# Kernel tuning notes

Measured on AMD Instinct MI355X. Metric: run time of the kernel, lower is better.

## Reference

```python
import jax, jax.numpy as jnp
import numpy as np

DECAY = 0.6
GAIN = 0.4
LN_EPS = 1e-5


def ema_scan(x, axis):
    # s_t = DECAY*s_{t-1} + GAIN*x_t, s_{-1}=0, along `axis`; vectorized over all other dims
    xm = jnp.moveaxis(x, axis, 0)
    def step(s, xt):
        s = DECAY * s + GAIN * xt
        return s, s
    _, ys = jax.lax.scan(step, jnp.zeros_like(xm[0]), xm)
    return jnp.moveaxis(ys, 0, axis)


def setup_inputs() -> dict:
    key = jax.random.key(0)
    ks = jax.random.split(key, 8)
    B, H, W, D = 8, 96, 96, 192
    C = 2 * D  # inner_dim
    s_in = 1.0 / np.sqrt(D)
    s_out = 1.0 / np.sqrt(C)
    return {
        "x": jax.random.normal(ks[0], (B, H, W, D), dtype=jnp.float32),
        "W_in": jax.random.uniform(ks[1], (D, C), minval=-s_in, maxval=s_in, dtype=jnp.float32),
        "b_in": jax.random.uniform(ks[2], (C,), minval=-s_in, maxval=s_in, dtype=jnp.float32),
        "conv_w": jax.random.uniform(ks[3], (C, 1, 3, 3), minval=-1.0/3.0, maxval=1.0/3.0, dtype=jnp.float32),
        "ln_g": jnp.ones((C,), dtype=jnp.float32),
        "ln_b": jnp.zeros((C,), dtype=jnp.float32),
        "W_out": jax.random.uniform(ks[4], (C, D), minval=-s_out, maxval=s_out, dtype=jnp.float32),
        "b_out": jax.random.uniform(ks[5], (D,), minval=-s_out, maxval=s_out, dtype=jnp.float32),
    }


def reference(x, W_in, b_in, conv_w, ln_g, ln_b, W_out, b_out):
    C = W_in.shape[1]
    # in_proj: [B,H,W,D] -> [B,H,W,C]
    proj = jnp.einsum("bhwd,dc->bhwc", x, W_in) + b_in
    # channels-first for depthwise conv: [B,C,H,W]
    cf = jnp.transpose(proj, (0, 3, 1, 2))
    local = jax.lax.conv_general_dilated(
        cf, conv_w, window_strides=(1, 1), padding="SAME",
        feature_group_count=C,
        dimension_numbers=("NCHW", "OIHW", "NCHW"))
    # four directional EMA scans
    lr = ema_scan(local, 3)
    rl = jnp.flip(ema_scan(jnp.flip(local, 3), 3), 3)
    tb = ema_scan(local, 2)
    bt = jnp.flip(ema_scan(jnp.flip(local, 2), 2), 2)
    mixed = 0.25 * (lr + rl + tb + bt) + local
    # back to channels-last, layernorm over C
    mixed = jnp.transpose(mixed, (0, 2, 3, 1))
    mu = jnp.mean(mixed, axis=-1, keepdims=True)
    var = jnp.mean(jnp.square(mixed - mu), axis=-1, keepdims=True)
    normed = (mixed - mu) * jax.lax.rsqrt(var + LN_EPS) * ln_g + ln_b
    return jnp.einsum("bhwc,cd->bhwd", normed, W_out) + b_out
```

## Files before the change

### kernel.cpp

```cpp
#include <hip/hip_runtime.h>
#include <hip/hip_bf16.h>

#define NB 8
#define NH 96
#define NW 96
#define ND 192
#define NC 384
#define NPOS (NB*NH*NW)

#define DECAY 0.6f
#define GAIN 0.4f
#define D12 2.1767823e-3f
#define D16 2.8211099e-4f
#define D24 4.7383813e-6f

typedef __attribute__((ext_vector_type(8))) short bf16x8;
typedef __attribute__((ext_vector_type(4))) float f32x4;
typedef __attribute__((ext_vector_type(4))) unsigned short us4;

__device__ inline unsigned short f2bf(float f) {
  unsigned u = __float_as_uint(f);
  u += 0x7fff + ((u >> 16) & 1);
  return (unsigned short)(u >> 16);
}
__device__ inline float bf2f(unsigned short u) {
  return __uint_as_float((unsigned)u << 16);
}

__device__ inline void gload16(const void* g, void* l) {
  __builtin_amdgcn_global_load_lds(
      (const __attribute__((address_space(1))) void*)g,
      (__attribute__((address_space(3))) void*)l, 16, 0, 0);
}

__device__ inline f32x4 ldf4(const float* p) {
  return *reinterpret_cast<const f32x4*>(p);
}
__device__ inline f32x4 ldb4(const unsigned short* p) {
  us4 v = *reinterpret_cast<const us4*>(p);
  return (f32x4){bf2f(v.x), bf2f(v.y), bf2f(v.z), bf2f(v.w)};
}
__device__ inline void stb4(unsigned short* p, f32x4 v) {
  us4 o = {f2bf(v[0]), f2bf(v[1]), f2bf(v[2]), f2bf(v[3])};
  *reinterpret_cast<us4*>(p) = o;
}
__device__ inline uint2 pk4(f32x4 v) {
  us4 o = {f2bf(v[0]), f2bf(v[1]), f2bf(v[2]), f2bf(v[3])};
  uint2 r; __builtin_memcpy(&r, &o, 8); return r;
}
__device__ inline f32x4 up4(uint2 p) {
  return (f32x4){__uint_as_float(p.x << 16), __uint_as_float(p.x & 0xffff0000u),
                 __uint_as_float(p.y << 16), __uint_as_float(p.y & 0xffff0000u)};
}
__device__ inline bf16x8 pk8(f32x4 a, f32x4 b) {
  bf16x8 r;
#pragma unroll
  for (int i = 0; i < 4; ++i) {
    r[i]     = (short)f2bf(a[i]);
    r[i + 4] = (short)f2bf(b[i]);
  }
  return r;
}
__device__ inline unsigned mswz(int row, int byteInRow) {
  return (unsigned)(row * 768 + (byteInRow ^ ((row & 7) << 4)));
}

__global__ __launch_bounds__(256) void cvt_w_kernel(
    const float* __restrict__ Wi, const float* __restrict__ Wo,
    unsigned short* __restrict__ WtI, unsigned short* __restrict__ WtO) {
  int idx = blockIdx.x * 256 + threadIdx.x;
  if (idx < ND * NC) {
    int k = idx / NC, c = idx % NC;
    WtI[c * ND + k] = f2bf(Wi[idx]);
  } else {
    int j = idx - ND * NC;
    int k = j / ND, d = j % ND;
    WtO[d * NC + k] = f2bf(Wo[j]);
  }
}

template<int K, int N, int BN>
__global__ __launch_bounds__(256) void gemm_kernel(
    const float* __restrict__ A32,
    const unsigned short* __restrict__ Bt,
    const float* __restrict__ bias,
    unsigned short* __restrict__ C) {
  constexpr int NF = BN / 32;
  __shared__ __align__(16) unsigned short lsA[8192];
  __shared__ __align__(16) unsigned short lsB[4 * BN * 8];

  const int tid = threadIdx.x;
  const int lane = tid & 63;
  const int wid = tid >> 6;
  const int wm = wid >> 1, wn = wid & 1;
  const int kg = lane >> 4, r16 = lane & 15;
  const int m0 = blockIdx.x * 128;
  const int n0 = blockIdx.y * BN;

  const float* srcAf[4]; float* dstAf[4];
  {
    float* lsAf = (float*)lsA;
#pragma unroll
    for (int p = 0; p < 4; ++p) {
      int s = tid + p * 256;
      int row = s >> 3, g = s & 7;
      int gg = g ^ (row & 7);
      srcAf[p] = A32 + (size_t)(m0 + row) * K + gg * 4;
      dstAf[p] = lsAf + s * 4;
    }
  }
  const unsigned short* srcB0 = Bt + (size_t)(n0 + (tid & (BN - 1))) * K + (tid / BN) * 8;
  const int sb1 = tid + 256;
  const unsigned short* srcBh = Bt + (size_t)(n0 + (sb1 & 127)) * K + (sb1 >> 7) * 8;

  int boff[NF];
#pragma unroll
  for (int n = 0; n < NF; ++n)
    boff[n] = (kg * BN + wn * (BN / 2) + n * 16 + r16) * 8;

  f32x4 acc[4][NF];
  float bv[NF];
#pragma unroll
  for (int n = 0; n < NF; ++n) bv[n] = bias[n0 + wn * (BN / 2) + n * 16 + r16];
#pragma unroll
  for (int m = 0; m < 4; ++m)
#pragma unroll
    for (int n = 0; n < NF; ++n)
      acc[m][n] = (f32x4){bv[n], bv[n], bv[n], bv[n]};

  for (int ks = 0; ks < K / 32; ++ks) {
    const int ke = ks * 32;
#pragma unroll
    for (int p = 0; p < 4; ++p) gload16(srcAf[p] + ke, dstAf[p]);
    gload16(srcB0 + ke, &lsB[tid * 8]);
    if constexpr (BN == 128) gload16(srcBh + ke, &lsB[(tid + 256) * 8]);
    __syncthreads();
    bf16x8 af[4], bfr[NF];
    {
      const float* lsAf = (const float*)lsA;
      const int r7 = r16 & 7;
#pragma unroll
      for (int m = 0; m < 4; ++m) {
        const int rowf = wm * 64 + m * 16 + r16;
        const float* rp = lsAf + rowf * 32;
        f32x4 a0 = *reinterpret_cast<const f32x4*>(rp + ((2 * kg) ^ r7) * 4);
        f32x4 a1 = *reinterpret_cast<const f32x4*>(rp + ((2 * kg + 1) ^ r7) * 4);
        af[m] = pk8(a0, a1);
      }
    }
#pragma unroll
    for (int n = 0; n < NF; ++n)
      bfr[n] = *reinterpret_cast<const bf16x8*>(&lsB[boff[n]]);
#pragma unroll
    for (int m = 0; m < 4; ++m)
#pragma unroll
      for (int n = 0; n < NF; ++n)
        acc[m][n] = __builtin_amdgcn_mfma_f32_16x16x32_bf16(af[m], bfr[n], acc[m][n], 0, 0, 0);
    __syncthreads();
  }

#pragma unroll
  for (int m = 0; m < 4; ++m) {
    const int row = m0 + wm * 64 + m * 16 + kg * 4;
#pragma unroll
    for (int n = 0; n < NF; ++n) {
      const int col = n0 + wn * (BN / 2) + n * 16 + r16;
#pragma unroll
      for (int j = 0; j < 4; ++j)
        C[(size_t)(row + j) * N + col] = f2bf(acc[m][n][j]);
    }
  }
}

__global__ __launch_bounds__(576) void dh_kernel(
    const unsigned short* __restrict__ proj, const float* __restrict__ cw,
    unsigned short* __restrict__ loc_t, unsigned short* __restrict__ acc_t) {
  __shared__ f32x4 agf[6][96];
  __shared__ f32x4 agb[6][96];
  const int tid = threadIdx.x;
  const int c4 = tid % 96;
  const int seg = tid / 96;
  const int w0 = seg * 16;
  const int bid = blockIdx.x;
  const int bh = (bid & 7) * NH + (bid >> 3);
  const int h = bh % NH;
  const int b = bh / NH;

  f32x4 raw[9];
  const float* cwp = cw + (size_t)c4 * 36;
#pragma unroll
  for (int i = 0; i < 9; ++i) raw[i] = ldf4(cwp + i * 4);
  f32x4 qq[9];
#pragma unroll
  for (int tap = 0; tap < 9; ++tap)
#pragma unroll
    for (int c = 0; c < 4; ++c)
      qq[tap][c] = raw[(c * 9 + tap) >> 2][(c * 9 + tap) & 3];

  const bool hm = (h > 0), hp = (h < NH - 1);
  const unsigned short* rowm = proj + ((size_t)(bh - 1) * NW) * NC + c4 * 4;
  const unsigned short* rowc = proj + ((size_t)bh * NW) * NC + c4 * 4;
  const unsigned short* rowp = proj + ((size_t)(bh + 1) * NW) * NC + c4 * 4;
  unsigned short* tbase = loc_t + ((size_t)(b * NW + w0) * NH + h) * NC + c4 * 4;
  unsigned short* abase = acc_t + ((size_t)(b * NW + w0) * NH + h) * NC + c4 * 4;
  const size_t wst = (size_t)NH * NC;

  const f32x4 z = {0.f, 0.f, 0.f, 0.f};
  f32x4 colL[3], colC[3], colR[3];
  if (w0 > 0) {
    colL[0] = hm ? ldb4(rowm + (size_t)(w0 - 1) * NC) : z;
    colL[1] = ldb4(rowc + (size_t)(w0 - 1) * NC);
    colL[2] = hp ? ldb4(rowp + (size_t)(w0 - 1) * NC) : z;
  } else { colL[0] = z; colL[1] = z; colL[2] = z; }
  colC[0] = hm ? ldb4(rowm + (size_t)w0 * NC) : z;
  colC[1] = ldb4(rowc + (size_t)w0 * NC);
  colC[2] = hp ? ldb4(rowp + (size_t)w0 * NC) : z;

  uint2 xr[16];
#pragma unroll
  for (int i = 0; i < 16; ++i) {
    const int w = w0 + i;
    if (w + 1 < NW) {
      colR[0] = hm ? ldb4(rowm + (size_t)(w + 1) * NC) : z;
      colR[1] = ldb4(rowc + (size_t)(w + 1) * NC);
      colR[2] = hp ? ldb4(rowp + (size_t)(w + 1) * NC) : z;
    } else { colR[0] = z; colR[1] = z; colR[2] = z; }
    f32x4 a = colL[0] * qq[0] + colC[0] * qq[1] + colR[0] * qq[2]
            + colL[1] * qq[3] + colC[1] * qq[4] + colR[1] * qq[5]
            + colL[2] * qq[6] + colC[2] * qq[7] + colR[2] * qq[8];
    xr[i] = pk4(a);
    *reinterpret_cast<uint2*>(tbase + (size_t)i * wst) = xr[i];
    colL[0] = colC[0]; colL[1] = colC[1]; colL[2] = colC[2];
    colC[0] = colR[0]; colC[1] = colR[1]; colC[2] = colR[2];
  }

  f32x4 Af = z, Ab = z;
#pragma unroll
  for (int i = 0; i < 16; ++i) Af = DECAY * Af + GAIN * up4(xr[i]);
#pragma unroll
  for (int i = 15; i >= 0; --i) Ab = DECAY * Ab + GAIN * up4(xr[i]);
  agf[seg][c4] = Af; agb[seg][c4] = Ab;
  __syncthreads();
  f32x4 Fin = z, Bin = z;
  if (seg >= 1) Fin = agf[seg - 1][c4];
  if (seg >= 2) Fin += D16 * agf[seg - 2][c4];
  if (seg <= 4) Bin = agb[seg + 1][c4];
  if (seg <= 3) Bin += D16 * agb[seg + 2][c4];

  uint2 bwp[16];
  f32x4 Bs = Bin;
#pragma unroll
  for (int i = 15; i >= 0; --i) {
    Bs = DECAY * Bs + GAIN * up4(xr[i]);
    bwp[i] = pk4(Bs);
  }
  f32x4 Fs = Fin;
#pragma unroll
  for (int i = 0; i < 16; ++i) {
    Fs = DECAY * Fs + GAIN * up4(xr[i]);
    stb4(abase + (size_t)i * wst, Fs + up4(bwp[i]));
  }
}

__global__ __launch_bounds__(768) void vgemm_kernel(
    const unsigned short* __restrict__ loc_t, const unsigned short* __restrict__ acc_t,
    const float* __restrict__ g, const float* __restrict__ bb,
    const unsigned short* __restrict__ WtO, const float* __restrict__ bo,
    float* __restrict__ out) {
  __shared__ __align__(16) unsigned short mix[96 * NC];
  __shared__ __align__(16) unsigned short lsB[2][6144];
  f32x4* ag = (f32x4*)mix;
  char* mixc = (char*)mix;
  const int tid = threadIdx.x;
  const int lane = tid & 63;
  const int kg = lane >> 4, r16 = lane & 15;
  const int c4 = tid % 96;
  const int seg = tid / 96;
  const int h0 = seg * 12;
  const int bw = blockIdx.x;

  {
    int d = tid % 192, kgg = tid / 192;
    gload16(WtO + (size_t)d * NC + kgg * 8, &lsB[0][tid * 8]);
  }

  const size_t base = ((size_t)bw * NH + h0) * NC + c4 * 4;
  const unsigned short* lp = loc_t + base;
  const unsigned short* ap = acc_t + base;
  uint2 xr[12], tp[12];
#pragma unroll
  for (int i = 0; i < 12; ++i) xr[i] = *reinterpret_cast<const uint2*>(lp + (size_t)i * NC);
#pragma unroll
  for (int i = 0; i < 12; ++i) tp[i] = *reinterpret_cast<const uint2*>(ap + (size_t)i * NC);

  const f32x4 z = {0.f, 0.f, 0.f, 0.f};
  f32x4 Bs = z, Fs = z;
#pragma unroll
  for (int i = 11; i >= 0; --i) {
    f32x4 xv = up4(xr[i]);
    Bs = DECAY * Bs + GAIN * xv;
    tp[i] = pk4(xv + 0.25f * (up4(tp[i]) + Bs));
  }
#pragma unroll
  for (int i = 0; i < 12; ++i) {
    Fs = DECAY * Fs + GAIN * up4(xr[i]);
    tp[i] = pk4(up4(tp[i]) + 0.25f * Fs);
  }
  ag[seg * 96 + c4] = Fs;
  ag[768 + seg * 96 + c4] = Bs;
  __syncthreads();
  f32x4 Fin = z, Bin = z;
  if (seg >= 1) Fin = ag[(seg - 1) * 96 + c4];
  if (seg >= 2) Fin += D12 * ag[(seg - 2) * 96 + c4];
  if (seg >= 3) Fin += D24 * ag[(seg - 3) * 96 + c4];
  if (seg <= 6) Bin = ag[768 + (seg + 1) * 96 + c4];
  if (seg <= 5) Bin += D12 * ag[768 + (seg + 2) * 96 + c4];
  if (seg <= 4) Bin += D24 * ag[768 + (seg + 3) * 96 + c4];
  __syncthreads();

  {
    const float dpw[12] = {0.6f, 0.36f, 0.216f, 0.1296f, 0.07776f, 0.046656f,
                           0.0279936f, 0.01679616f, 0.010077696f,
                           0.0060466176f, 0.0036279706f, 0.0021767823f};
#pragma unroll
    for (int i = 0; i < 12; ++i) {
      f32x4 mx = up4(tp[i]) + 0.25f * (dpw[i] * Fin + dpw[11 - i] * Bin);
      stb4((unsigned short*)(mixc + mswz(h0 + i, c4 * 8)), mx);
    }
  }
  __syncthreads();

  const int wave = tid >> 6;
  const int cb = lane * 6;
  {
    float gv[6], bv6[6];
#pragma unroll
    for (int i = 0; i < 6; ++i) { gv[i] = g[cb + i]; bv6[i] = bb[cb + i]; }
    for (int h = wave; h < NH; h += 12) {
      ushort2* p0 = (ushort2*)(mixc + mswz(h, lane * 12));
      ushort2* p1 = (ushort2*)(mixc + mswz(h, lane * 12 + 4));
      ushort2* p2 = (ushort2*)(mixc + mswz(h, lane * 12 + 8));
      ushort2 a2 = *p0, b2 = *p1, c2 = *p2;
      float v[6];
      v[0] = bf2f(a2.x); v[1] = bf2f(a2.y);
      v[2] = bf2f(b2.x); v[3] = bf2f(b2.y);
      v[4] = bf2f(c2.x); v[5] = bf2f(c2.y);
      float sm = 0.f, s2 = 0.f;
#pragma unroll
      for (int i = 0; i < 6; ++i) { sm += v[i]; s2 += v[i] * v[i]; }
#pragma unroll
      for (int o = 32; o > 0; o >>= 1) {
        sm += __shfl_xor(sm, o, 64);
        s2 += __shfl_xor(s2, o, 64);
      }
      float mu = sm * (1.f / NC);
      float r = rsqrtf(s2 * (1.f / NC) - mu * mu + 1e-5f);
      unsigned short o6[6];
#pragma unroll
      for (int i = 0; i < 6; ++i)
        o6[i] = f2bf((v[i] - mu) * r * gv[i] + bv6[i]);
      *p0 = (ushort2){o6[0], o6[1]};
      *p1 = (ushort2){o6[2], o6[3]};
      *p2 = (ushort2){o6[4], o6[5]};
    }
  }
  __syncthreads();

  const int wm = wave >> 2, wn = wave & 3;
  f32x4 acc[2][3];
  {
    float bv[3];
#pragma unroll
    for (int n = 0; n < 3; ++n) bv[n] = bo[wn * 48 + n * 16 + r16];
#pragma unroll
    for (int m = 0; m < 2; ++m)
#pragma unroll
      for (int n = 0; n < 3; ++n)
        acc[m][n] = (f32x4){bv[n], bv[n], bv[n], bv[n]};
  }
  for (int ks = 0; ks < 12; ++ks) {
    if (ks < 11) {
      int d = tid % 192, kgg = tid / 192;
      gload16(WtO + (size_t)d * NC + (ks + 1) * 32 + kgg * 8, &lsB[(ks + 1) & 1][tid * 8]);
    }
    const unsigned short* bufp = lsB[ks & 1];
    bf16x8 af[2], bfr[3];
#pragma unroll
    for (int m = 0; m < 2; ++m) {
      const int row = wm * 32 + m * 16 + r16;
      af[m] = *reinterpret_cast<const bf16x8*>(mixc + mswz(row, ks * 64 + kg * 16));
    }
#pragma unroll
    for (int n = 0; n < 3; ++n)
      bfr[n] = *reinterpret_cast<const bf16x8*>(&bufp[(kg * 192 + wn * 48 + n * 16 + r16) * 8]);
#pragma unroll
    for (int m = 0; m < 2; ++m)
#pragma unroll
      for (int n = 0; n < 3; ++n)
        acc[m][n] = __builtin_amdgcn_mfma_f32_16x16x32_bf16(af[m], bfr[n], acc[m][n], 0, 0, 0);
    __syncthreads();
  }

  const int bq = bw / NW, wq = bw % NW;
#pragma unroll
  for (int m = 0; m < 2; ++m) {
    const int hbase = wm * 32 + m * 16 + kg * 4;
#pragma unroll
    for (int n = 0; n < 3; ++n) {
      const int d = wn * 48 + n * 16 + r16;
#pragma unroll
      for (int j = 0; j < 4; ++j)
        out[((size_t)(bq * NH + hbase + j) * NW + wq) * ND + d] = acc[m][n][j];
    }
  }
}

extern "C" void kernel_launch(void* const* d_in, const int* in_sizes, int n_in,
                              void* d_out, int out_size, void* d_ws, size_t ws_size,
                              hipStream_t stream) {
  const float* x    = (const float*)d_in[0];
  const float* W_in = (const float*)d_in[1];
  const float* b_in = (const float*)d_in[2];
  const float* cw   = (const float*)d_in[3];
  const float* ln_g = (const float*)d_in[4];
  const float* ln_b = (const float*)d_in[5];
  const float* W_out= (const float*)d_in[6];
  const float* b_out= (const float*)d_in[7];
  float* out = (float*)d_out;

  unsigned short* wsu   = (unsigned short*)d_ws;
  unsigned short* proj  = wsu;
  unsigned short* loc_t = proj + 28311552;
  unsigned short* acc_t = loc_t + 28311552;
  unsigned short* WtI   = acc_t + 28311552;
  unsigned short* WtO   = WtI + 73728;

  cvt_w_kernel<<<(2 * ND * NC) / 256, 256, 0, stream>>>(W_in, W_out, WtI, WtO);
  {
    dim3 g(NPOS / 128, NC / 128);
    gemm_kernel<ND, NC, 128><<<g, 256, 0, stream>>>(x, WtI, b_in, proj);
  }
  dh_kernel<<<NB * NH, 576, 0, stream>>>(proj, cw, loc_t, acc_t);
  vgemm_kernel<<<NB * NW, 768, 0, stream>>>(loc_t, acc_t, ln_g, ln_b,
                                            WtO, b_out, out);
}
```

Baseline: 190.3 us.

## Split vgemm column scan into two half-column blocks with recomputed boundary carries

Each (batch, column) in the vertical-scan + layernorm + out-proj kernel is now handled by two blocks, one per 48-row half, instead of one block covering all 96 rows. The carry from the other half is approximated by re-scanning the three nearest 6-row segments of the opposite half and truncating older contributions. LDS use per block is halved and the grid doubles, aiming for more blocks resident per CU and better latency hiding. The cost is extra redundant loads and scan work at the boundary, a truncated carry (decay^18 tail dropped), and a smaller MFMA tile per wave.

```diff
diff --git a/kernel.cpp b/kernel.cpp
--- a/kernel.cpp
+++ b/kernel.cpp
@@ -10,9 +10,9 @@
 
 #define DECAY 0.6f
 #define GAIN 0.4f
+#define D6  4.6656e-2f
 #define D12 2.1767823e-3f
 #define D16 2.8211099e-4f
-#define D24 4.7383813e-6f
 
 typedef __attribute__((ext_vector_type(8))) short bf16x8;
 typedef __attribute__((ext_vector_type(4))) float f32x4;
@@ -262,70 +262,88 @@
   }
 }
 
-__global__ __launch_bounds__(768) void vgemm_kernel(
+__global__ __launch_bounds__(768, 6) void vgemm_kernel(
     const unsigned short* __restrict__ loc_t, const unsigned short* __restrict__ acc_t,
     const float* __restrict__ g, const float* __restrict__ bb,
     const unsigned short* __restrict__ WtO, const float* __restrict__ bo,
     float* __restrict__ out) {
-  __shared__ __align__(16) unsigned short mix[96 * NC];
+  __shared__ __align__(16) unsigned short mix[48 * NC];
   __shared__ __align__(16) unsigned short lsB[2][6144];
-  f32x4* ag = (f32x4*)mix;
+  f32x4* AGF = (f32x4*)mix;
+  f32x4* AGB = AGF + 12 * 96;
   char* mixc = (char*)mix;
   const int tid = threadIdx.x;
   const int lane = tid & 63;
   const int kg = lane >> 4, r16 = lane & 15;
   const int c4 = tid % 96;
   const int seg = tid / 96;
-  const int h0 = seg * 12;
-  const int bw = blockIdx.x;
+  const int bx = blockIdx.x;
+  const int half = bx & 1;
+  const int bw = bx >> 1;
 
   {
     int d = tid % 192, kgg = tid / 192;
     gload16(WtO + (size_t)d * NC + kgg * 8, &lsB[0][tid * 8]);
   }
 
-  const size_t base = ((size_t)bw * NH + h0) * NC + c4 * 4;
+  const int r0 = half * 48 + seg * 6;
+  const size_t base = ((size_t)bw * NH + r0) * NC + c4 * 4;
   const unsigned short* lp = loc_t + base;
   const unsigned short* ap = acc_t + base;
-  uint2 xr[12], tp[12];
-#pragma unroll
-  for (int i = 0; i < 12; ++i) xr[i] = *reinterpret_cast<const uint2*>(lp + (size_t)i * NC);
-#pragma unroll
-  for (int i = 0; i < 12; ++i) tp[i] = *reinterpret_cast<const uint2*>(ap + (size_t)i * NC);
+  uint2 xr[6], tp[6];
+#pragma unroll
+  for (int i = 0; i < 6; ++i) xr[i] = *reinterpret_cast<const uint2*>(lp + (size_t)i * NC);
+#pragma unroll
+  for (int i = 0; i < 6; ++i) tp[i] = *reinterpret_cast<const uint2*>(ap + (size_t)i * NC);
 
   const f32x4 z = {0.f, 0.f, 0.f, 0.f};
   f32x4 Bs = z, Fs = z;
 #pragma unroll
-  for (int i = 11; i >= 0; --i) {
+  for (int i = 5; i >= 0; --i) {
     f32x4 xv = up4(xr[i]);
     Bs = DECAY * Bs + GAIN * xv;
     tp[i] = pk4(xv + 0.25f * (up4(tp[i]) + Bs));
   }
 #pragma unroll
-  for (int i = 0; i < 12; ++i) {
+  for (int i = 0; i < 6; ++i) {
     Fs = DECAY * Fs + GAIN * up4(xr[i]);
     tp[i] = pk4(up4(tp[i]) + 0.25f * Fs);
   }
-  ag[seg * 96 + c4] = Fs;
-  ag[768 + seg * 96 + c4] = Bs;
+  AGF[(seg + 3) * 96 + c4] = Fs;
+  AGB[seg * 96 + c4] = Bs;
+
+  if (tid < 288) {
+    const int ws = seg;
+    const int wr0 = half ? (30 + ws * 6) : (48 + ws * 6);
+    const unsigned short* wp = loc_t + ((size_t)bw * NH + wr0) * NC + c4 * 4;
+    f32x4 wa = z;
+    if (half) {
+#pragma unroll
+      for (int i = 0; i < 6; ++i)
+        wa = DECAY * wa + GAIN * up4(*reinterpret_cast<const uint2*>(wp + (size_t)i * NC));
+      AGF[ws * 96 + c4] = wa;
+      AGB[(8 + ws) * 96 + c4] = z;
+    } else {
+#pragma unroll
+      for (int i = 5; i >= 0; --i)
+        wa = DECAY * wa + GAIN * up4(*reinterpret_cast<const uint2*>(wp + (size_t)i * NC));
+      AGB[(8 + ws) * 96 + c4] = wa;
+      AGF[ws * 96 + c4] = z;
+    }
+  }
   __syncthreads();
-  f32x4 Fin = z, Bin = z;
-  if (seg >= 1) Fin = ag[(seg - 1) * 96 + c4];
-  if (seg >= 2) Fin += D12 * ag[(seg - 2) * 96 + c4];
-  if (seg >= 3) Fin += D24 * ag[(seg - 3) * 96 + c4];
-  if (seg <= 6) Bin = ag[768 + (seg + 1) * 96 + c4];
-  if (seg <= 5) Bin += D12 * ag[768 + (seg + 2) * 96 + c4];
-  if (seg <= 4) Bin += D24 * ag[768 + (seg + 3) * 96 + c4];
+  f32x4 Fin = AGF[(seg + 2) * 96 + c4] + D6 * AGF[(seg + 1) * 96 + c4]
+            + D12 * AGF[seg * 96 + c4];
+  f32x4 Bin = AGB[(seg + 1) * 96 + c4] + D6 * AGB[(seg + 2) * 96 + c4]
+            + D12 * AGB[(seg + 3) * 96 + c4];
   __syncthreads();
 
   {
-    const float dpw[12] = {0.6f, 0.36f, 0.216f, 0.1296f, 0.07776f, 0.046656f,
-                           0.0279936f, 0.01679616f, 0.010077696f,
-                           0.0060466176f, 0.0036279706f, 0.0021767823f};
-#pragma unroll
-    for (int i = 0; i < 12; ++i) {
-      f32x4 mx = up4(tp[i]) + 0.25f * (dpw[i] * Fin + dpw[11 - i] * Bin);
-      stb4((unsigned short*)(mixc + mswz(h0 + i, c4 * 8)), mx);
+    const float dpw[6] = {0.6f, 0.36f, 0.216f, 0.1296f, 0.07776f, 0.046656f};
+#pragma unroll
+    for (int i = 0; i < 6; ++i) {
+      f32x4 mx = up4(tp[i]) + 0.25f * (dpw[i] * Fin + dpw[5 - i] * Bin);
+      stb4((unsigned short*)(mixc + mswz(seg * 6 + i, c4 * 8)), mx);
     }
   }
   __syncthreads();
@@ -336,7 +354,7 @@
     float gv[6], bv6[6];
 #pragma unroll
     for (int i = 0; i < 6; ++i) { gv[i] = g[cb + i]; bv6[i] = bb[cb + i]; }
-    for (int h = wave; h < NH; h += 12) {
+    for (int h = wave; h < 48; h += 12) {
       ushort2* p0 = (ushort2*)(mixc + mswz(h, lane * 12));
       ushort2* p1 = (ushort2*)(mixc + mswz(h, lane * 12 + 4));
       ushort2* p2 = (ushort2*)(mixc + mswz(h, lane * 12 + 8));
@@ -367,16 +385,14 @@
   __syncthreads();
 
   const int wm = wave >> 2, wn = wave & 3;
-  f32x4 acc[2][3];
+  f32x4 acc[3];
   {
     float bv[3];
 #pragma unroll
     for (int n = 0; n < 3; ++n) bv[n] = bo[wn * 48 + n * 16 + r16];
 #pragma unroll
-    for (int m = 0; m < 2; ++m)
-#pragma unroll
-      for (int n = 0; n < 3; ++n)
-        acc[m][n] = (f32x4){bv[n], bv[n], bv[n], bv[n]};
+    for (int n = 0; n < 3; ++n)
+      acc[n] = (f32x4){bv[n], bv[n], bv[n], bv[n]};
   }
   for (int ks = 0; ks < 12; ++ks) {
     if (ks < 11) {
@@ -384,34 +400,25 @@
       gload16(WtO + (size_t)d * NC + (ks + 1) * 32 + kgg * 8, &lsB[(ks + 1) & 1][tid * 8]);
     }
     const unsigned short* bufp = lsB[ks & 1];
-    bf16x8 af[2], bfr[3];
-#pragma unroll
-    for (int m = 0; m < 2; ++m) {
-      const int row = wm * 32 + m * 16 + r16;
-      af[m] = *reinterpret_cast<const bf16x8*>(mixc + mswz(row, ks * 64 + kg * 16));
-    }
+    bf16x8 af, bfr[3];
+    af = *reinterpret_cast<const bf16x8*>(mixc + mswz(wm * 16 + r16, ks * 64 + kg * 16));
 #pragma unroll
     for (int n = 0; n < 3; ++n)
       bfr[n] = *reinterpret_cast<const bf16x8*>(&bufp[(kg * 192 + wn * 48 + n * 16 + r16) * 8]);
 #pragma unroll
-    for (int m = 0; m < 2; ++m)
-#pragma unroll
-      for (int n = 0; n < 3; ++n)
-        acc[m][n] = __builtin_amdgcn_mfma_f32_16x16x32_bf16(af[m], bfr[n], acc[m][n], 0, 0, 0);
+    for (int n = 0; n < 3; ++n)
+      acc[n] = __builtin_amdgcn_mfma_f32_16x16x32_bf16(af, bfr[n], acc[n], 0, 0, 0);
     __syncthreads();
   }
 
   const int bq = bw / NW, wq = bw % NW;
-#pragma unroll
-  for (int m = 0; m < 2; ++m) {
-    const int hbase = wm * 32 + m * 16 + kg * 4;
-#pragma unroll
-    for (int n = 0; n < 3; ++n) {
-      const int d = wn * 48 + n * 16 + r16;
-#pragma unroll
-      for (int j = 0; j < 4; ++j)
-        out[((size_t)(bq * NH + hbase + j) * NW + wq) * ND + d] = acc[m][n][j];
-    }
+  const int hbase = half * 48 + wm * 16 + kg * 4;
+#pragma unroll
+  for (int n = 0; n < 3; ++n) {
+    const int d = wn * 48 + n * 16 + r16;
+#pragma unroll
+    for (int j = 0; j < 4; ++j)
+      out[((size_t)(bq * NH + hbase + j) * NW + wq) * ND + d] = acc[n][j];
   }
 }
 
@@ -441,6 +448,6 @@
     gemm_kernel<ND, NC, 128><<<g, 256, 0, stream>>>(x, WtI, b_in, proj);
   }
   dh_kernel<<<NB * NH, 576, 0, stream>>>(proj, cw, loc_t, acc_t);
-  vgemm_kernel<<<NB * NW, 768, 0, stream>>>(loc_t, acc_t, ln_g, ln_b,
-                                            WtO, b_out, out);
-}
+  vgemm_kernel<<<NB * NW * 2, 768, 0, stream>>>(loc_t, acc_t, ln_g, ln_b,
+                                                WtO, b_out, out);
+}
```

Measured after the change: 204.8 us. +7.6%, slower.
